# Kernel optimization log

Measured on AMD Instinct MI355X. Metric: run time of the kernel, lower is better.

The kernel has to match this reference:

```python
import jax, jax.numpy as jnp
import numpy as np

NUM_HEADS = 16
HIDDEN = 1024
HEAD = HIDDEN // NUM_HEADS
NEG_INF = -10000.0


def setup_inputs() -> dict:
    key = jax.random.key(0)
    k1, k2, k3, k4 = jax.random.split(key, 4)
    B, S = 4, 2048
    x = jax.random.normal(k1, (B, S, HIDDEN), dtype=jnp.float32)
    pos_embeds = jax.random.normal(k2, (S, HIDDEN), dtype=jnp.float32)
    # Dense(3*hidden, use_bias=False) and Dense(hidden, use_bias=False)
    Wqkv = jax.random.normal(k3, (HIDDEN, 3 * HIDDEN), dtype=jnp.float32) / np.sqrt(HIDDEN)
    Wo = jax.random.normal(k4, (HIDDEN, HIDDEN), dtype=jnp.float32) / np.sqrt(HIDDEN)
    return {"x": x, "pos_embeds": pos_embeds, "Wqkv": Wqkv, "Wo": Wo}


def _compute_qkv(t, Wqkv):
    # rearrange '... s (k n h) -> k ... n s h', k=3, n=NUM_HEADS
    proj = t @ Wqkv  # [..., s, 3*n*h]
    proj = proj.reshape(*t.shape[:-1], 3, NUM_HEADS, HEAD)  # [..., s, 3, n, h]
    # move: k first, then leading dims, then n, s, h
    nd = proj.ndim
    perm = (nd - 3,) + tuple(range(nd - 4)) + (nd - 2, nd - 4, nd - 1)
    return jnp.transpose(proj, perm)  # [3, ..., n, s, h]


def reference(x, pos_embeds, Wqkv, Wo):
    S = x.shape[-2]
    q, k, v = _compute_qkv(x, Wqkv)  # each [B, n, S, h]
    pos_qkv = _compute_qkv(pos_embeds[:S], Wqkv)  # [3, n, S, h]
    pos_q, pos_k = pos_qkv[0], pos_qkv[1]
    q = q + pos_q  # broadcast over batch
    k = k + pos_k
    scores = jnp.einsum('bnqh,bnkh->bnqk', q, k) / np.sqrt(HEAD).astype(np.float32)
    causal = jnp.arange(S)[:, None] < jnp.arange(S)[None, :]  # strict upper triangle (future)
    scores = jnp.where(causal, NEG_INF, scores)
    probs = jax.nn.softmax(scores, axis=-1)
    # dropout deterministic (training=False) -> identity
    combined = jnp.einsum('bnqk,bnkh->bnqh', probs, v)  # [B, n, S, h]
    combined = jnp.transpose(combined, (0, 2, 1, 3)).reshape(x.shape[0], S, HIDDEN)  # '... n q h -> ... q (n h)'
    out = combined @ Wo
    return out
```

## Files before the change

### kernel.cpp

```cpp
#include <hip/hip_runtime.h>


typedef float f32x4 __attribute__((ext_vector_type(4)));
typedef short bf16x8 __attribute__((ext_vector_type(8)));
typedef short bf16x4 __attribute__((ext_vector_type(4)));

#define MFMA_BF16(a, b, c) __builtin_amdgcn_mfma_f32_16x16x32_bf16((a), (b), (c), 0, 0, 0)

#if __has_builtin(__builtin_amdgcn_mfma_f32_16x16x16bf16_1k)
#define HAVE_MFMA16 1
#define MFMA_BF16_K16(a, b, c) __builtin_amdgcn_mfma_f32_16x16x16bf16_1k((a), (b), (c), 0, 0, 0)
#else
#define HAVE_MFMA16 0
#endif

#define ASYNC_COPY16(lds, g)                                                   \
  __builtin_amdgcn_global_load_lds(                                            \
      (const __attribute__((address_space(1))) void*)(g),                      \
      (__attribute__((address_space(3))) void*)(lds), 16, 0, 0)

__device__ __forceinline__ short f2bf(float f) {
  union { float f; unsigned u; } v; v.f = f;
  unsigned u = v.u;
  u += 0x7fffu + ((u >> 16) & 1u);
  return (short)(u >> 16);
}

__device__ __forceinline__ float bf2f(short s) {
  union { unsigned u; float f; } v;
  v.u = ((unsigned)(unsigned short)s) << 16;
  return v.f;
}

__device__ __forceinline__ int pack_bf2_fast(float a, float b) {
  union { float f; unsigned u; } va, vb; va.f = a; vb.f = b;
  unsigned ua = va.u + 0x8000u;
  unsigned ub = vb.u + 0x8000u;
  return (int)((ua >> 16) | (ub & 0xffff0000u));
}

__device__ const int QT_X[30] = {5,6,7,8,9,10,11,11,12,12,13,13,14,14,15,15,
                                 4,10, 3,9,15, 2,8,14, 1,7,13, 0,6,12};
__device__ const int CH_X[30] = {0,0,0,0,0,0,0,1,0,1,0,1,0,1,0,1,
                                 0,1, 0,1,2, 0,1,2, 0,1,2, 0,1,2};
__device__ const int START_QT[16] = {0,1,2,3,4,5,6,8,10,12,14,16,18,21,24,27};

__global__ __launch_bounds__(256) void prep_x(const float* __restrict__ x,
                                              const float* __restrict__ pos,
                                              short* __restrict__ xb,
                                              short* __restrict__ xpb) {
  int i = blockIdx.x * 256 + threadIdx.x;
  int idx = i * 4;
  const float4 xv = *(const float4*)(x + idx);
  const float4 pv = *(const float4*)(pos + (idx & ((2048 * 1024) - 1)));
  short4 a, b;
  a.x = f2bf(xv.x); a.y = f2bf(xv.y); a.z = f2bf(xv.z); a.w = f2bf(xv.w);
  b.x = f2bf(xv.x + pv.x); b.y = f2bf(xv.y + pv.y);
  b.z = f2bf(xv.z + pv.z); b.w = f2bf(xv.w + pv.w);
  *(short4*)(xb + idx) = a;
  *(short4*)(xpb + idx) = b;
}

__global__ __launch_bounds__(256) void transpose_w(const float* __restrict__ in,
                                                   short* __restrict__ out,
                                                   int K, int N) {
  __shared__ float tile[32][33];
  int n0 = blockIdx.x * 32, k0 = blockIdx.y * 32;
  int c = threadIdx.x & 31, r0 = threadIdx.x >> 5;
  for (int i = 0; i < 4; i++) {
    int r = r0 + i * 8;
    tile[r][c] = in[(size_t)(k0 + r) * N + n0 + c];
  }
  __syncthreads();
  for (int i = 0; i < 4; i++) {
    int r = r0 + i * 8;
    out[(size_t)(n0 + r) * K + k0 + c] = f2bf(tile[c][r]);
  }
}

__global__ __launch_bounds__(256) void gemm_qkv(const short* __restrict__ xb,
                                                const short* __restrict__ xpb,
                                                const short* __restrict__ wt,
                                                short* __restrict__ qg,
                                                short* __restrict__ kg,
                                                short* __restrict__ vtg) {
  __shared__ __align__(16) short As[128 * 64];
  __shared__ __align__(16) short Bs[128 * 64];
  const int bm = blockIdx.x, bn = blockIdx.y;
  const short* __restrict__ A = (bn < 16) ? xpb : xb;
  const int tid = threadIdx.x;
  const int lane = tid & 63, w = tid >> 6;
  const int wm = w & 1, wn = w >> 1;
  const int quad = lane >> 4, l16 = lane & 15;
  const f32x4 fzero = {0.f, 0.f, 0.f, 0.f};
  f32x4 acc[4][4];
  for (int mt = 0; mt < 4; mt++)
    for (int nt = 0; nt < 4; nt++) acc[mt][nt] = fzero;
  const int arow0 = bm * 128, brow0 = bn * 128;
  const int swz8 = ((lane & 7) ^ (lane >> 3)) * 8;
  const short* gA = A + (size_t)(arow0 + w * 32 + (lane >> 3)) * 1024 + swz8;
  const short* gB = wt + (size_t)(brow0 + w * 32 + (lane >> 3)) * 1024 + swz8;
  char* ldsA = (char*)As + w * 4096;
  char* ldsB = (char*)Bs + w * 4096;

  for (int k0 = 0; k0 < 1024; k0 += 64) {
#pragma unroll
    for (int i = 0; i < 4; i++) {
      ASYNC_COPY16(ldsA + i * 1024, gA + i * 8192 + k0);
      ASYNC_COPY16(ldsB + i * 1024, gB + i * 8192 + k0);
    }
    __syncthreads();
#pragma unroll
    for (int ks = 0; ks < 2; ks++) {
      bf16x8 af[4], bfr[4];
#pragma unroll
      for (int mt = 0; mt < 4; mt++)
        af[mt] = *(const bf16x8*)(As + (wm * 64 + mt * 16 + l16) * 64 +
                                  (((ks * 4 + quad) ^ (l16 & 7)) * 8));
#pragma unroll
      for (int nt = 0; nt < 4; nt++)
        bfr[nt] = *(const bf16x8*)(Bs + (wn * 64 + nt * 16 + l16) * 64 +
                                   (((ks * 4 + quad) ^ (l16 & 7)) * 8));
#pragma unroll
      for (int mt = 0; mt < 4; mt++)
#pragma unroll
        for (int nt = 0; nt < 4; nt++)
          acc[mt][nt] = MFMA_BF16(af[mt], bfr[nt], acc[mt][nt]);
    }
    __syncthreads();
  }
  for (int nt = 0; nt < 4; nt++) {
    int col = bn * 128 + wn * 64 + nt * 16 + l16;
    int kk = col >> 10, head = (col >> 6) & 15, hh = col & 63;
    for (int mt = 0; mt < 4; mt++) {
      int rowb = bm * 128 + wm * 64 + mt * 16 + quad * 4;
      int b = rowb >> 11, s0 = rowb & 2047;
      if (kk == 2) {
        short4 sv;
        sv.x = f2bf(acc[mt][nt][0]); sv.y = f2bf(acc[mt][nt][1]);
        sv.z = f2bf(acc[mt][nt][2]); sv.w = f2bf(acc[mt][nt][3]);
        *(short4*)(vtg + (size_t)((b * 16 + head) * 64 + hh) * 2048 + s0) = sv;
      } else {
        short* __restrict__ dst = (kk == 0) ? qg : kg;
        float scale = (kk == 0) ? 0.18033688f : 1.0f;
        for (int r = 0; r < 4; r++)
          dst[(size_t)((b * 16 + head) * 2048 + s0 + r) * 64 + hh] =
              f2bf(acc[mt][nt][r] * scale);
      }
    }
  }
}

__global__ __launch_bounds__(256, 4) void attn_part(const short* __restrict__ qg,
                                                    const short* __restrict__ kg,
                                                    const short* __restrict__ vtg,
                                                    short* __restrict__ pO,
                                                    float* __restrict__ pL) {
  const int xi = blockIdx.x;
  const int qt = QT_X[xi], ch = CH_X[xi];
  const int head = blockIdx.y, b = blockIdx.z;
  const int bh = b * 16 + head;
  const int p = bh * 30 + START_QT[qt] + ch;
  const short* __restrict__ Q = qg + (size_t)bh * 2048 * 64;
  const short* __restrict__ K = kg + (size_t)bh * 2048 * 64;
  const short* __restrict__ VT = vtg + (size_t)bh * 64 * 2048;
  __shared__ __align__(16) short Ks[2][64 * 64];
  __shared__ __align__(16) short Vs[2][64 * 64];
#if !HAVE_MFMA16
  __shared__ __align__(16) short Ps[4][16 * 72];
#endif
  const int tid = threadIdx.x, lane = tid & 63, w = tid >> 6;
  const int quad = lane >> 4, l16 = lane & 15;
  const f32x4 fzero = {0.f, 0.f, 0.f, 0.f};

  bf16x8 bq[2][2];
#pragma unroll
  for (int sub = 0; sub < 2; sub++) {
    int qrow = qt * 128 + w * 32 + sub * 16 + l16;
#pragma unroll
    for (int ks = 0; ks < 2; ks++)
      bq[sub][ks] = *(const bf16x8*)(Q + (size_t)qrow * 64 + ks * 32 + quad * 8);
  }
  f32x4 acco[2][4];
  f32x4 lrun[2];
#pragma unroll
  for (int sub = 0; sub < 2; sub++) {
    for (int nt = 0; nt < 4; nt++) acco[sub][nt] = fzero;
    lrun[sub] = fzero;
  }

  const int kt0 = ch * 12;
  const int kt1 = min(kt0 + 12, 2 * qt + 2);
  const int qmin_w = qt * 128 + w * 32;

  const int sr0 = tid >> 3;
  const int sc0 = (tid & 7) * 8;
  const int swz = (((tid & 7) ^ (sr0 & 7)) * 8);
  const int o0 = sr0 * 64 + swz, o1 = (32 + sr0) * 64 + swz;

  int4 kreg[2], vreg[2];
  {
    int kv0 = kt0 * 64;
    kreg[0] = *(const int4*)(K + (size_t)(kv0 + sr0) * 64 + sc0);
    kreg[1] = *(const int4*)(K + (size_t)(kv0 + 32 + sr0) * 64 + sc0);
    vreg[0] = *(const int4*)(VT + (size_t)sr0 * 2048 + kv0 + sc0);
    vreg[1] = *(const int4*)(VT + (size_t)(32 + sr0) * 2048 + kv0 + sc0);
    *(int4*)(&Ks[0][o0]) = kreg[0];
    *(int4*)(&Ks[0][o1]) = kreg[1];
    *(int4*)(&Vs[0][o0]) = vreg[0];
    *(int4*)(&Vs[0][o1]) = vreg[1];
  }
  __syncthreads();

  for (int kt = kt0; kt < kt1; kt++) {
    const int cur = (kt - kt0) & 1;
    if (kt + 1 < kt1) {
      int kv0 = (kt + 1) * 64;
      kreg[0] = *(const int4*)(K + (size_t)(kv0 + sr0) * 64 + sc0);
      kreg[1] = *(const int4*)(K + (size_t)(kv0 + 32 + sr0) * 64 + sc0);
      vreg[0] = *(const int4*)(VT + (size_t)sr0 * 2048 + kv0 + sc0);
      vreg[1] = *(const int4*)(VT + (size_t)(32 + sr0) * 2048 + kv0 + sc0);
    }

    if (kt * 64 <= qmin_w + 31) {
      f32x4 accs[2][4];
#pragma unroll
      for (int sub = 0; sub < 2; sub++)
        for (int nt = 0; nt < 4; nt++) accs[sub][nt] = fzero;
#pragma unroll
      for (int ks = 0; ks < 2; ks++)
#pragma unroll
        for (int nt = 0; nt < 4; nt++) {
          bf16x8 ak = *(const bf16x8*)(&Ks[cur][(nt * 16 + l16) * 64 +
                                               (((ks * 4 + quad) ^ (l16 & 7)) * 8)]);
          accs[0][nt] = MFMA_BF16(ak, bq[0][ks], accs[0][nt]);
          accs[1][nt] = MFMA_BF16(ak, bq[1][ks], accs[1][nt]);
        }

      if ((kt + 1) * 64 > qmin_w) {
#pragma unroll
        for (int sub = 0; sub < 2; sub++) {
          int q = qmin_w + sub * 16 + l16;
#pragma unroll
          for (int nt = 0; nt < 4; nt++) {
            int kv = kt * 64 + nt * 16 + quad * 4;
#pragma unroll
            for (int r = 0; r < 4; r++)
              if (kv + r > q) accs[sub][nt][r] = -1e30f;
          }
        }
      }

#pragma unroll
      for (int sub = 0; sub < 2; sub++)
#pragma unroll
        for (int nt = 0; nt < 4; nt++) {
#pragma unroll
          for (int r = 0; r < 4; r++) accs[sub][nt][r] = exp2f(accs[sub][nt][r]);
          lrun[sub] += accs[sub][nt];
        }

#if HAVE_MFMA16
#pragma unroll
      for (int kk = 0; kk < 4; kk++) {
        union { int2 i2; bf16x4 v; } p0, p1;
        p0.i2.x = pack_bf2_fast(accs[0][kk][0], accs[0][kk][1]);
        p0.i2.y = pack_bf2_fast(accs[0][kk][2], accs[0][kk][3]);
        p1.i2.x = pack_bf2_fast(accs[1][kk][0], accs[1][kk][1]);
        p1.i2.y = pack_bf2_fast(accs[1][kk][2], accs[1][kk][3]);
#pragma unroll
        for (int nth = 0; nth < 4; nth++) {
          bf16x4 av = *(const bf16x4*)(&Vs[cur][(nth * 16 + l16) * 64 +
                                               (((kk * 2 + (quad >> 1)) ^ (l16 & 7)) * 8) +
                                               (quad & 1) * 4]);
          acco[0][nth] = MFMA_BF16_K16(av, p0.v, acco[0][nth]);
          acco[1][nth] = MFMA_BF16_K16(av, p1.v, acco[1][nth]);
        }
      }
#else
      short* P = Ps[w];
#pragma unroll
      for (int sub = 0; sub < 2; sub++) {
#pragma unroll
        for (int nt = 0; nt < 4; nt++) {
          int2 pk;
          pk.x = pack_bf2_fast(accs[sub][nt][0], accs[sub][nt][1]);
          pk.y = pack_bf2_fast(accs[sub][nt][2], accs[sub][nt][3]);
          *(int2*)(P + l16 * 72 + nt * 16 + quad * 4) = pk;
        }
#pragma unroll
        for (int ks2 = 0; ks2 < 2; ks2++) {
          bf16x8 bp = *(const bf16x8*)(P + l16 * 72 + ks2 * 32 + quad * 8);
#pragma unroll
          for (int nth = 0; nth < 4; nth++) {
            bf16x8 av = *(const bf16x8*)(&Vs[cur][(nth * 16 + l16) * 64 +
                                                 (((ks2 * 4 + quad) ^ (l16 & 7)) * 8)]);
            acco[sub][nth] = MFMA_BF16(av, bp, acco[sub][nth]);
          }
        }
      }
#endif
    }

    if (kt + 1 < kt1) {
      const int nxt = cur ^ 1;
      *(int4*)(&Ks[nxt][o0]) = kreg[0];
      *(int4*)(&Ks[nxt][o1]) = kreg[1];
      *(int4*)(&Vs[nxt][o0]) = vreg[0];
      *(int4*)(&Vs[nxt][o1]) = vreg[1];
    }
    __syncthreads();
  }

#pragma unroll
  for (int sub = 0; sub < 2; sub++) {
    float lh = (lrun[sub][0] + lrun[sub][1]) + (lrun[sub][2] + lrun[sub][3]);
    lh += __shfl_xor(lh, 16);
    lh += __shfl_xor(lh, 32);
    int qloc = w * 32 + sub * 16 + l16;
    if (quad == 0) pL[p * 128 + qloc] = lh;
    size_t base = (size_t)p * 8192 + (size_t)qloc * 64;
#pragma unroll
    for (int nth = 0; nth < 4; nth++) {
      short4 sv;
      sv.x = f2bf(acco[sub][nth][0]);
      sv.y = f2bf(acco[sub][nth][1]);
      sv.z = f2bf(acco[sub][nth][2]);
      sv.w = f2bf(acco[sub][nth][3]);
      *(short4*)(pO + base + nth * 16 + quad * 4) = sv;
    }
  }
}

__global__ __launch_bounds__(256) void attn_merge(const short* __restrict__ pO,
                                                  const float* __restrict__ pL,
                                                  short* __restrict__ comb) {
  const int qt = blockIdx.x, head = blockIdx.y, b = blockIdx.z;
  const int bh = b * 16 + head;
  const int nch = (2 * qt + 13) / 12;
  const int p0 = bh * 30 + START_QT[qt];
  const int t = threadIdx.x;
  const int qloc = t >> 1, hh = (t & 1) * 32;

  float l = 0.f;
  for (int c = 0; c < nch; c++) l += pL[(p0 + c) * 128 + qloc];
  const float inv = 1.f / l;

  float acc[32];
#pragma unroll
  for (int j = 0; j < 32; j++) acc[j] = 0.f;
  for (int c = 0; c < nch; c++) {
    const short* src = pO + (size_t)(p0 + c) * 8192 + (size_t)qloc * 64 + hh;
#pragma unroll
    for (int v = 0; v < 4; v++) {
      short4 d0 = *(const short4*)(src + v * 8);
      short4 d1 = *(const short4*)(src + v * 8 + 4);
      acc[v * 8 + 0] += bf2f(d0.x); acc[v * 8 + 1] += bf2f(d0.y);
      acc[v * 8 + 2] += bf2f(d0.z); acc[v * 8 + 3] += bf2f(d0.w);
      acc[v * 8 + 4] += bf2f(d1.x); acc[v * 8 + 5] += bf2f(d1.y);
      acc[v * 8 + 6] += bf2f(d1.z); acc[v * 8 + 7] += bf2f(d1.w);
    }
  }
  size_t base = (size_t)(b * 2048 + qt * 128 + qloc) * 1024 + head * 64 + hh;
#pragma unroll
  for (int v = 0; v < 8; v++) {
    short4 sv;
    sv.x = f2bf(acc[v * 4 + 0] * inv);
    sv.y = f2bf(acc[v * 4 + 1] * inv);
    sv.z = f2bf(acc[v * 4 + 2] * inv);
    sv.w = f2bf(acc[v * 4 + 3] * inv);
    *(short4*)(comb + base + v * 4) = sv;
  }
}

__global__ __launch_bounds__(256) void gemm_out(const short* __restrict__ A,
                                                const short* __restrict__ wt,
                                                float* __restrict__ out) {
  __shared__ __align__(16) short As[128 * 64];
  __shared__ __align__(16) short Bs[128 * 64];
  const int bm = blockIdx.x, bn = blockIdx.y;
  const int tid = threadIdx.x;
  const int lane = tid & 63, w = tid >> 6;
  const int wm = w & 1, wn = w >> 1;
  const int quad = lane >> 4, l16 = lane & 15;
  const f32x4 fzero = {0.f, 0.f, 0.f, 0.f};
  f32x4 acc[4][4];
  for (int mt = 0; mt < 4; mt++)
    for (int nt = 0; nt < 4; nt++) acc[mt][nt] = fzero;
  const int arow0 = bm * 128, brow0 = bn * 128;
  const int swz8 = ((lane & 7) ^ (lane >> 3)) * 8;
  const short* gA = A + (size_t)(arow0 + w * 32 + (lane >> 3)) * 1024 + swz8;
  const short* gB = wt + (size_t)(brow0 + w * 32 + (lane >> 3)) * 1024 + swz8;
  char* ldsA = (char*)As + w * 4096;
  char* ldsB = (char*)Bs + w * 4096;

  for (int k0 = 0; k0 < 1024; k0 += 64) {
#pragma unroll
    for (int i = 0; i < 4; i++) {
      ASYNC_COPY16(ldsA + i * 1024, gA + i * 8192 + k0);
      ASYNC_COPY16(ldsB + i * 1024, gB + i * 8192 + k0);
    }
    __syncthreads();
#pragma unroll
    for (int ks = 0; ks < 2; ks++) {
      bf16x8 af[4], bfr[4];
#pragma unroll
      for (int mt = 0; mt < 4; mt++)
        af[mt] = *(const bf16x8*)(As + (wm * 64 + mt * 16 + l16) * 64 +
                                  (((ks * 4 + quad) ^ (l16 & 7)) * 8));
#pragma unroll
      for (int nt = 0; nt < 4; nt++)
        bfr[nt] = *(const bf16x8*)(Bs + (wn * 64 + nt * 16 + l16) * 64 +
                                   (((ks * 4 + quad) ^ (l16 & 7)) * 8));
#pragma unroll
      for (int mt = 0; mt < 4; mt++)
#pragma unroll
        for (int nt = 0; nt < 4; nt++)
          acc[mt][nt] = MFMA_BF16(af[mt], bfr[nt], acc[mt][nt]);
    }
    __syncthreads();
  }
  for (int nt = 0; nt < 4; nt++) {
    int col = bn * 128 + wn * 64 + nt * 16 + l16;
    for (int mt = 0; mt < 4; mt++) {
      int rowb = bm * 128 + wm * 64 + mt * 16 + quad * 4;
      for (int r = 0; r < 4; r++)
        out[(size_t)(rowb + r) * 1024 + col] = acc[mt][nt][r];
    }
  }
}

extern "C" void kernel_launch(void* const* d_in, const int* in_sizes, int n_in,
                              void* d_out, int out_size, void* d_ws, size_t ws_size,
                              hipStream_t stream) {
  const float* x    = (const float*)d_in[0];
  const float* pos  = (const float*)d_in[1];
  const float* Wqkv = (const float*)d_in[2];
  const float* Wo   = (const float*)d_in[3];
  float* out = (float*)d_out;

  char* ws = (char*)d_ws;
  const size_t SZ = (size_t)8192 * 1024 * 2;
  short* xb    = (short*)(ws);
  short* xpb   = (short*)(ws + SZ);
  short* pO    = (short*)(ws);
  float* pL    = (float*)(ws + (size_t)1920 * 8192 * 2);
  short* q     = (short*)(ws + 2 * SZ);
  short* k     = (short*)(ws + 3 * SZ);
  short* vt    = (short*)(ws + 4 * SZ);
  short* comb  = (short*)(ws + 5 * SZ);
  short* wqkvt = (short*)(ws + 6 * SZ);
  short* wot   = (short*)(ws + 6 * SZ + (size_t)3072 * 1024 * 2);

  prep_x<<<8192, 256, 0, stream>>>(x, pos, xb, xpb);
  transpose_w<<<dim3(96, 32), 256, 0, stream>>>(Wqkv, wqkvt, 1024, 3072);
  transpose_w<<<dim3(32, 32), 256, 0, stream>>>(Wo, wot, 1024, 1024);
  gemm_qkv<<<dim3(64, 24), 256, 0, stream>>>(xb, xpb, wqkvt, q, k, vt);
  attn_part<<<dim3(30, 16, 4), 256, 0, stream>>>(q, k, vt, pO, pL);
  attn_merge<<<dim3(16, 16, 4), 256, 0, stream>>>(pO, pL, comb);
  gemm_out<<<dim3(64, 8), 256, 0, stream>>>(comb, wot, out);
}
```

Before: 326.1 us.

## Use async global-to-LDS copies in attention and vectorize Q/K epilogue stores

Attention K/V tile loads now go straight from global memory to LDS through the async copy path instead of being staged in registers and stored by hand. This frees registers, so the occupancy hint is raised from 4 to 5 blocks. In the QKV GEMM, the Q/K tiles swap the MFMA operand order so each lane holds 4 consecutive head dims, which lets the epilogue write short4 vectors instead of scattered scalar bf16 stores. The risk is that the prefetch into the other buffer now overlaps with compute on the current buffer, and correctness depends on the single sync per iteration and on the async copies completing in time.

Result: slower. 383.4 us (+17.6%).

```diff
diff --git a/kernel.cpp b/kernel.cpp
--- a/kernel.cpp
+++ b/kernel.cpp
@@ -87,7 +87,8 @@
   __shared__ __align__(16) short As[128 * 64];
   __shared__ __align__(16) short Bs[128 * 64];
   const int bm = blockIdx.x, bn = blockIdx.y;
-  const short* __restrict__ A = (bn < 16) ? xpb : xb;
+  const bool is_v = (bn >= 16);
+  const short* __restrict__ A = is_v ? xb : xpb;
   const int tid = threadIdx.x;
   const int lane = tid & 63, w = tid >> 6;
   const int wm = w & 1, wn = w >> 1;
@@ -121,37 +122,56 @@
       for (int nt = 0; nt < 4; nt++)
         bfr[nt] = *(const bf16x8*)(Bs + (wn * 64 + nt * 16 + l16) * 64 +
                                    (((ks * 4 + quad) ^ (l16 & 7)) * 8));
-#pragma unroll
-      for (int mt = 0; mt < 4; mt++)
-#pragma unroll
-        for (int nt = 0; nt < 4; nt++)
-          acc[mt][nt] = MFMA_BF16(af[mt], bfr[nt], acc[mt][nt]);
+      if (is_v) {
+#pragma unroll
+        for (int mt = 0; mt < 4; mt++)
+#pragma unroll
+          for (int nt = 0; nt < 4; nt++)
+            acc[mt][nt] = MFMA_BF16(af[mt], bfr[nt], acc[mt][nt]);
+      } else {
+#pragma unroll
+        for (int mt = 0; mt < 4; mt++)
+#pragma unroll
+          for (int nt = 0; nt < 4; nt++)
+            acc[mt][nt] = MFMA_BF16(bfr[nt], af[mt], acc[mt][nt]);
+      }
     }
     __syncthreads();
   }
-  for (int nt = 0; nt < 4; nt++) {
-    int col = bn * 128 + wn * 64 + nt * 16 + l16;
-    int kk = col >> 10, head = (col >> 6) & 15, hh = col & 63;
-    for (int mt = 0; mt < 4; mt++) {
-      int rowb = bm * 128 + wm * 64 + mt * 16 + quad * 4;
-      int b = rowb >> 11, s0 = rowb & 2047;
-      if (kk == 2) {
+  if (is_v) {
+    for (int nt = 0; nt < 4; nt++) {
+      int col = brow0 + wn * 64 + nt * 16 + l16;
+      int head = (col >> 6) & 15, hh = col & 63;
+      for (int mt = 0; mt < 4; mt++) {
+        int rowb = arow0 + wm * 64 + mt * 16 + quad * 4;
+        int b = rowb >> 11, s0 = rowb & 2047;
         short4 sv;
         sv.x = f2bf(acc[mt][nt][0]); sv.y = f2bf(acc[mt][nt][1]);
         sv.z = f2bf(acc[mt][nt][2]); sv.w = f2bf(acc[mt][nt][3]);
         *(short4*)(vtg + (size_t)((b * 16 + head) * 64 + hh) * 2048 + s0) = sv;
-      } else {
+      }
+    }
+  } else {
+    for (int mt = 0; mt < 4; mt++) {
+      int srow = arow0 + wm * 64 + mt * 16 + l16;
+      int b = srow >> 11, s0 = srow & 2047;
+      for (int nt = 0; nt < 4; nt++) {
+        int n = brow0 + wn * 64 + nt * 16 + quad * 4;
+        int kk = n >> 10, head = (n >> 6) & 15, hh = n & 63;
         short* __restrict__ dst = (kk == 0) ? qg : kg;
         float scale = (kk == 0) ? 0.18033688f : 1.0f;
-        for (int r = 0; r < 4; r++)
-          dst[(size_t)((b * 16 + head) * 2048 + s0 + r) * 64 + hh] =
-              f2bf(acc[mt][nt][r] * scale);
-      }
-    }
-  }
-}
-
-__global__ __launch_bounds__(256, 4) void attn_part(const short* __restrict__ qg,
+        short4 sv;
+        sv.x = f2bf(acc[mt][nt][0] * scale);
+        sv.y = f2bf(acc[mt][nt][1] * scale);
+        sv.z = f2bf(acc[mt][nt][2] * scale);
+        sv.w = f2bf(acc[mt][nt][3] * scale);
+        *(short4*)(dst + (size_t)((b * 16 + head) * 2048 + s0) * 64 + hh) = sv;
+      }
+    }
+  }
+}
+
+__global__ __launch_bounds__(256, 5) void attn_part(const short* __restrict__ qg,
                                                     const short* __restrict__ kg,
                                                     const short* __restrict__ vtg,
                                                     short* __restrict__ pO,
@@ -193,33 +213,30 @@
   const int kt1 = min(kt0 + 12, 2 * qt + 2);
   const int qmin_w = qt * 128 + w * 32;
 
-  const int sr0 = tid >> 3;
-  const int sc0 = (tid & 7) * 8;
-  const int swz = (((tid & 7) ^ (sr0 & 7)) * 8);
-  const int o0 = sr0 * 64 + swz, o1 = (32 + sr0) * 64 + swz;
-
-  int4 kreg[2], vreg[2];
+  const int swz8 = ((lane & 7) ^ (lane >> 3)) * 8;
+  const short* gK = K + (size_t)(w * 16 + (lane >> 3)) * 64 + swz8;
+  const short* gV0 = VT + (size_t)(w * 16 + (lane >> 3)) * 2048 + swz8;
+  const short* gV1 = VT + (size_t)(w * 16 + 8 + (lane >> 3)) * 2048 + swz8;
+  const int ldsO = w * 2048;
+
   {
     int kv0 = kt0 * 64;
-    kreg[0] = *(const int4*)(K + (size_t)(kv0 + sr0) * 64 + sc0);
-    kreg[1] = *(const int4*)(K + (size_t)(kv0 + 32 + sr0) * 64 + sc0);
-    vreg[0] = *(const int4*)(VT + (size_t)sr0 * 2048 + kv0 + sc0);
-    vreg[1] = *(const int4*)(VT + (size_t)(32 + sr0) * 2048 + kv0 + sc0);
-    *(int4*)(&Ks[0][o0]) = kreg[0];
-    *(int4*)(&Ks[0][o1]) = kreg[1];
-    *(int4*)(&Vs[0][o0]) = vreg[0];
-    *(int4*)(&Vs[0][o1]) = vreg[1];
+    ASYNC_COPY16((char*)Ks[0] + ldsO, gK + (size_t)kv0 * 64);
+    ASYNC_COPY16((char*)Ks[0] + ldsO + 1024, gK + (size_t)kv0 * 64 + 8 * 64);
+    ASYNC_COPY16((char*)Vs[0] + ldsO, gV0 + kv0);
+    ASYNC_COPY16((char*)Vs[0] + ldsO + 1024, gV1 + kv0);
   }
   __syncthreads();
 
   for (int kt = kt0; kt < kt1; kt++) {
     const int cur = (kt - kt0) & 1;
     if (kt + 1 < kt1) {
+      const int nxt = cur ^ 1;
       int kv0 = (kt + 1) * 64;
-      kreg[0] = *(const int4*)(K + (size_t)(kv0 + sr0) * 64 + sc0);
-      kreg[1] = *(const int4*)(K + (size_t)(kv0 + 32 + sr0) * 64 + sc0);
-      vreg[0] = *(const int4*)(VT + (size_t)sr0 * 2048 + kv0 + sc0);
-      vreg[1] = *(const int4*)(VT + (size_t)(32 + sr0) * 2048 + kv0 + sc0);
+      ASYNC_COPY16((char*)Ks[nxt] + ldsO, gK + (size_t)kv0 * 64);
+      ASYNC_COPY16((char*)Ks[nxt] + ldsO + 1024, gK + (size_t)kv0 * 64 + 8 * 64);
+      ASYNC_COPY16((char*)Vs[nxt] + ldsO, gV0 + kv0);
+      ASYNC_COPY16((char*)Vs[nxt] + ldsO + 1024, gV1 + kv0);
     }
 
     if (kt * 64 <= qmin_w + 31) {
@@ -300,14 +317,6 @@
         }
       }
 #endif
-    }
-
-    if (kt + 1 < kt1) {
-      const int nxt = cur ^ 1;
-      *(int4*)(&Ks[nxt][o0]) = kreg[0];
-      *(int4*)(&Ks[nxt][o1]) = kreg[1];
-      *(int4*)(&Vs[nxt][o0]) = vreg[0];
-      *(int4*)(&Vs[nxt][o1]) = vreg[1];
     }
     __syncthreads();
   }
```
